# Optimization experiments

Hardware: AMD Instinct MI355X
Metric: run time of the kernel (lower is better)

Reference implementation:

```python
import jax, jax.numpy as jnp
import numpy as np

D_MODEL = 1024
N_HEADS = 16
HEAD_DIM = D_MODEL // N_HEADS
BATCH = 4
SEQ = 2048


def setup_inputs() -> dict:
    key = jax.random.key(0)
    ks = jax.random.split(key, 5)
    # Xavier uniform bound for square d_model x d_model weights
    bound = np.sqrt(6.0 / (D_MODEL + D_MODEL))
    x = jax.random.normal(ks[0], (BATCH, SEQ, D_MODEL), dtype=jnp.float32)
    attention_mask = jnp.ones((BATCH, SEQ), dtype=jnp.int32)
    wq = jax.random.uniform(ks[1], (D_MODEL, D_MODEL), jnp.float32, -bound, bound)
    wk = jax.random.uniform(ks[2], (D_MODEL, D_MODEL), jnp.float32, -bound, bound)
    wv = jax.random.uniform(ks[3], (D_MODEL, D_MODEL), jnp.float32, -bound, bound)
    wo = jax.random.uniform(ks[4], (D_MODEL, D_MODEL), jnp.float32, -bound, bound)
    return {"x": x, "attention_mask": attention_mask,
            "wq": wq, "wk": wk, "wv": wv, "wo": wo}


def reference(x, attention_mask, wq, wk, wv, wo):
    # x: (B, S, D). Linear weights stored torch-style (out, in): y = x @ W^T
    B, S, D = x.shape
    H, Hd = N_HEADS, HEAD_DIM
    scale = np.sqrt(Hd).astype(np.float32)

    def split_heads(t):  # (B,S,D) -> (B,H,S,Hd)
        return t.reshape(B, S, H, Hd).transpose(0, 2, 1, 3)

    q = split_heads(jnp.einsum('bsd,ed->bse', x, wq))
    k = split_heads(jnp.einsum('bsd,ed->bse', x, wk))
    v = split_heads(jnp.einsum('bsd,ed->bse', x, wv))

    scores = jnp.einsum('bhqd,bhkd->bhqk', q, k) / scale  # (B,H,S,S)

    causal = jnp.tril(jnp.ones((S, S), dtype=bool))  # True = keep
    keep = causal[None, None, :, :] & (attention_mask[:, None, None, :] != 0)
    scores = jnp.where(keep, scores, -jnp.inf)

    attn = jax.nn.softmax(scores, axis=-1)  # dropout: eval mode (identity)
    out = jnp.einsum('bhqk,bhkd->bhqd', attn, v)  # (B,H,S,Hd)
    out = out.transpose(0, 2, 1, 3).reshape(B, S, D)
    return jnp.einsum('bsd,ed->bse', out, wo)
```

## Files before the change

kernel.cpp:

```cpp
#include <hip/hip_runtime.h>
#include <cstdint>
#include <cstddef>

#define D_MODEL 1024
#define N_HEADS 16
#define HEAD_DIM 64
#define BATCH 4
#define SEQ 2048
#define M_TOTAL (BATCH * SEQ)

typedef __attribute__((ext_vector_type(8))) short bf16x8;
typedef __attribute__((ext_vector_type(4))) float f32x4;
typedef __attribute__((ext_vector_type(16))) float f32x16;

#define Q_SCALE 0.18033688011112042f

__device__ __forceinline__ unsigned short f2bu(float f) {
    union { float f; unsigned u; } x; x.f = f;
    unsigned r = x.u + 0x7FFFu + ((x.u >> 16) & 1u);
    return (unsigned short)(r >> 16);
}

__device__ __forceinline__ void async16(void* lds, const void* g) {
    __builtin_amdgcn_global_load_lds(
        (const __attribute__((address_space(1))) void*)g,
        (__attribute__((address_space(3))) void*)lds, 16, 0, 0);
}

__global__ __launch_bounds__(256) void cast_all(const float* __restrict__ x,
                                                const float* __restrict__ wq,
                                                const float* __restrict__ wk,
                                                const float* __restrict__ wv,
                                                const float* __restrict__ wo,
                                                unsigned short* __restrict__ dst) {
    const size_t NE = (size_t)M_TOTAL * D_MODEL;
    const size_t WE = (size_t)D_MODEL * D_MODEL;
    size_t i4 = (size_t)blockIdx.x * 256 + threadIdx.x;
    size_t e = i4 * 4;
    const float* src; size_t off;
    if (e < NE) { src = x; off = e; }
    else {
        size_t t = e - NE;
        int r = (int)(t / WE); off = t - (size_t)r * WE;
        src = (r == 0) ? wq : (r == 1) ? wk : (r == 2) ? wv : wo;
    }
    float4 v = *(const float4*)(src + off);
    ushort4 o;
    o.x = f2bu(v.x); o.y = f2bu(v.y); o.z = f2bu(v.z); o.w = f2bu(v.w);
    ((ushort4*)dst)[i4] = o;
}

__global__ __launch_bounds__(256) void qkv_gemm(const unsigned short* __restrict__ X,
                                                const unsigned short* __restrict__ W0,
                                                const unsigned short* __restrict__ W1,
                                                const unsigned short* __restrict__ W2,
                                                unsigned short* __restrict__ Y0,
                                                unsigned short* __restrict__ Y1,
                                                unsigned short* __restrict__ Vt) {
    __shared__ short As[128 * 32];
    __shared__ short Bs[128 * 32];

    const int sel = blockIdx.x >> 3;
    const unsigned short* W = (sel == 0) ? W0 : (sel == 1) ? W1 : W2;
    const float scl = (sel == 0) ? Q_SCALE : 1.0f;

    const int tid = threadIdx.x;
    const int w = tid >> 6, lane = tid & 63, quad = lane >> 4, l15 = lane & 15;
    const int wm = w & 1, wn = w >> 1;
    const int rowBase = blockIdx.y * 128;
    const int colBase = (blockIdx.x & 7) * 128;

    f32x4 acc[4][4];
#pragma unroll
    for (int mi = 0; mi < 4; ++mi)
#pragma unroll
        for (int ni = 0; ni < 4; ++ni)
#pragma unroll
            for (int e = 0; e < 4; ++e) acc[mi][ni][e] = 0.f;

    for (int k0 = 0; k0 < 1024; k0 += 32) {
        __syncthreads();
#pragma unroll
        for (int l = 0; l < 2; ++l) {
            int c = tid + l * 256;
            int row = c >> 2, ccs = c & 3;
            int cc = ccs ^ ((row >> 1) & 3);
            async16((char*)As + c * 16, X + (size_t)(rowBase + row) * 1024 + k0 + cc * 8);
            async16((char*)Bs + c * 16, W + (size_t)(colBase + row) * 1024 + k0 + cc * 8);
        }
        __syncthreads();

        bf16x8 a[4], b[4];
#pragma unroll
        for (int mi = 0; mi < 4; ++mi) {
            int r = wm * 64 + mi * 16 + l15;
            int slot = quad ^ ((r >> 1) & 3);
            a[mi] = *(const bf16x8*)&As[r * 32 + slot * 8];
        }
#pragma unroll
        for (int ni = 0; ni < 4; ++ni) {
            int r = wn * 64 + ni * 16 + l15;
            int slot = quad ^ ((r >> 1) & 3);
            b[ni] = *(const bf16x8*)&Bs[r * 32 + slot * 8];
        }
#pragma unroll
        for (int mi = 0; mi < 4; ++mi)
#pragma unroll
            for (int ni = 0; ni < 4; ++ni)
                acc[mi][ni] = __builtin_amdgcn_mfma_f32_16x16x32_bf16(a[mi], b[ni], acc[mi][ni], 0, 0, 0);
    }

    if (sel != 2) {
        unsigned short* Y = (sel == 0) ? Y0 : Y1;
#pragma unroll
        for (int mi = 0; mi < 4; ++mi)
#pragma unroll
            for (int ni = 0; ni < 4; ++ni)
#pragma unroll
                for (int reg = 0; reg < 4; ++reg) {
                    int row = rowBase + wm * 64 + mi * 16 + quad * 4 + reg;
                    int col = colBase + wn * 64 + ni * 16 + l15;
                    Y[(size_t)row * 1024 + col] = f2bu(acc[mi][ni][reg] * scl);
                }
    } else {
#pragma unroll
        for (int mi = 0; mi < 4; ++mi) {
            int row0 = rowBase + wm * 64 + mi * 16 + quad * 4;
            int bb = row0 >> 11;
            int s0 = row0 & 2047;
#pragma unroll
            for (int ni = 0; ni < 4; ++ni) {
                int col = colBase + wn * 64 + ni * 16 + l15;
                int hh = col >> 6, dd = col & 63;
                ushort4 pk;
                pk.x = f2bu(acc[mi][ni][0]); pk.y = f2bu(acc[mi][ni][1]);
                pk.z = f2bu(acc[mi][ni][2]); pk.w = f2bu(acc[mi][ni][3]);
                *(ushort4*)(Vt + (((size_t)bb * 16 + hh) * 64 + dd) * SEQ + s0) = pk;
            }
        }
    }
}

__global__ __launch_bounds__(256) void out_gemm(const unsigned short* __restrict__ X,
                                                const unsigned short* __restrict__ W,
                                                float* __restrict__ Y) {
    __shared__ short As[128 * 32];
    __shared__ short Bs[128 * 32];

    const int tid = threadIdx.x;
    const int w = tid >> 6, lane = tid & 63, quad = lane >> 4, l15 = lane & 15;
    const int wm = w & 1, wn = w >> 1;
    const int rowBase = blockIdx.y * 128;
    const int colBase = blockIdx.x * 128;

    f32x4 acc[4][4];
#pragma unroll
    for (int mi = 0; mi < 4; ++mi)
#pragma unroll
        for (int ni = 0; ni < 4; ++ni)
#pragma unroll
            for (int e = 0; e < 4; ++e) acc[mi][ni][e] = 0.f;

    for (int k0 = 0; k0 < 1024; k0 += 32) {
        __syncthreads();
#pragma unroll
        for (int l = 0; l < 2; ++l) {
            int c = tid + l * 256;
            int row = c >> 2, ccs = c & 3;
            int cc = ccs ^ ((row >> 1) & 3);
            async16((char*)As + c * 16, X + (size_t)(rowBase + row) * 1024 + k0 + cc * 8);
            async16((char*)Bs + c * 16, W + (size_t)(colBase + row) * 1024 + k0 + cc * 8);
        }
        __syncthreads();

        bf16x8 a[4], b[4];
#pragma unroll
        for (int mi = 0; mi < 4; ++mi) {
            int r = wm * 64 + mi * 16 + l15;
            int slot = quad ^ ((r >> 1) & 3);
            a[mi] = *(const bf16x8*)&As[r * 32 + slot * 8];
        }
#pragma unroll
        for (int ni = 0; ni < 4; ++ni) {
            int r = wn * 64 + ni * 16 + l15;
            int slot = quad ^ ((r >> 1) & 3);
            b[ni] = *(const bf16x8*)&Bs[r * 32 + slot * 8];
        }
#pragma unroll
        for (int mi = 0; mi < 4; ++mi)
#pragma unroll
            for (int ni = 0; ni < 4; ++ni)
                acc[mi][ni] = __builtin_amdgcn_mfma_f32_16x16x32_bf16(a[mi], b[ni], acc[mi][ni], 0, 0, 0);
    }

#pragma unroll
    for (int mi = 0; mi < 4; ++mi)
#pragma unroll
        for (int ni = 0; ni < 4; ++ni)
#pragma unroll
            for (int reg = 0; reg < 4; ++reg) {
                int row = rowBase + wm * 64 + mi * 16 + quad * 4 + reg;
                int col = colBase + wn * 64 + ni * 16 + l15;
                Y[(size_t)row * 1024 + col] = acc[mi][ni][reg];
            }
}

__global__ __launch_bounds__(256) void flash32(const unsigned short* __restrict__ Q,
                                               const unsigned short* __restrict__ K,
                                               const unsigned short* __restrict__ Vt,
                                               const int* __restrict__ mask,
                                               unsigned short* __restrict__ CTX) {
    __shared__ short lds[16384];
    __shared__ float biasS[2][64];
    __shared__ int allokS[2];
    __shared__ int okW[4];

    const int bh = blockIdx.x;
    const int qt = 15 - (int)blockIdx.y;
    const int b = bh >> 4;
    const int tid = threadIdx.x;
    const int w = tid >> 6, lane = tid & 63, l31 = lane & 31, lane5 = lane >> 5;

    const size_t qkBase = (size_t)b * SEQ * D_MODEL + (size_t)(bh & 15) * HEAD_DIM;
    const size_t vtBase = (size_t)bh * HEAD_DIM * SEQ;

    {
        int ok = 1;
        for (int i = tid; i < SEQ; i += 256) ok &= (mask[b * SEQ + i] != 0);
        unsigned long long bal = __ballot(ok != 0);
        if (lane == 0) okW[w] = (bal == ~0ull) ? 1 : 0;
    }
    __syncthreads();
    const int allSeq = okW[0] & okW[1] & okW[2] & okW[3];

    int stp[2], stcc[2], stj[2];
#pragma unroll
    for (int l = 0; l < 2; ++l) {
        int c = tid + l * 256;
        int p = c >> 3, sl = c & 7;
        stp[l] = p;
        stcc[l] = sl ^ (p & 7);
        stj[l] = (p & 0x33) | ((p & 4) << 1) | ((p & 8) >> 1);
    }

    const int q0 = qt * 128;
    const int iq = q0 + w * 32 + l31;

    bf16x8 qf[4];
#pragma unroll
    for (int ks = 0; ks < 4; ++ks)
        qf[ks] = *(const bf16x8*)(Q + qkBase + (size_t)iq * D_MODEL + ks * 16 + lane5 * 8);

    float mv = -INFINITY, lv = 0.f;
    f32x16 Ot[2];
#pragma unroll
    for (int dt = 0; dt < 2; ++dt)
#pragma unroll
        for (int e = 0; e < 16; ++e) Ot[dt][e] = 0.f;

    const int ktmax = 2 * qt + 1;

    uint4 kreg[2], vreg[2];
    int mreg = 1;
#pragma unroll
    for (int l = 0; l < 2; ++l) {
        kreg[l] = *(const uint4*)(K + qkBase + (size_t)stj[l] * D_MODEL + stcc[l] * 8);
        vreg[l] = *(const uint4*)(Vt + vtBase + (size_t)stp[l] * SEQ + stcc[l] * 8);
    }
    if (!allSeq && tid < 64) mreg = mask[b * SEQ + tid];

    for (int kt = 0; kt <= ktmax; ++kt) {
        const int k0 = kt * 64;
        const int buf = kt & 1;
#pragma unroll
        for (int l = 0; l < 2; ++l) {
            int c = tid + l * 256;
            *(uint4*)((char*)lds + buf * 8192 + c * 16) = kreg[l];
            *(uint4*)((char*)lds + 16384 + buf * 8192 + c * 16) = vreg[l];
        }
        if (!allSeq && tid < 64) {
            biasS[buf][tid] = mreg ? 0.f : -INFINITY;
            unsigned long long bal = __ballot(mreg != 0);
            if (tid == 0) allokS[buf] = (bal == ~0ull) ? 1 : 0;
        }
        if (kt < ktmax) {
            const int kn = k0 + 64;
#pragma unroll
            for (int l = 0; l < 2; ++l) {
                kreg[l] = *(const uint4*)(K + qkBase + (size_t)(kn + stj[l]) * D_MODEL + stcc[l] * 8);
                vreg[l] = *(const uint4*)(Vt + vtBase + (size_t)stp[l] * SEQ + kn + stcc[l] * 8);
            }
            if (!allSeq && tid < 64) mreg = mask[b * SEQ + kn + tid];
        }
        __syncthreads();

        if (64 * kt > q0 + 32 * w + 31) continue;

        const short* Ks = lds + buf * 4096;
        const short* Vs = lds + 8192 + buf * 4096;

        f32x16 St[2];
#pragma unroll
        for (int T = 0; T < 2; ++T)
#pragma unroll
            for (int e = 0; e < 16; ++e) St[T][e] = 0.f;
        __builtin_amdgcn_s_setprio(1);
#pragma unroll
        for (int T = 0; T < 2; ++T)
#pragma unroll
            for (int ks = 0; ks < 4; ++ks) {
                int p = T * 32 + l31;
                int slot = (ks * 2 + lane5) ^ (p & 7);
                bf16x8 a = *(const bf16x8*)&Ks[p * 64 + slot * 8];
                St[T] = __builtin_amdgcn_mfma_f32_32x32x16_bf16(a, qf[ks], St[T], 0, 0, 0);
            }
        __builtin_amdgcn_s_setprio(0);

        const bool partial = (k0 + 63 > q0 + 32 * w);
        if (partial) {
#pragma unroll
            for (int T = 0; T < 2; ++T)
#pragma unroll
                for (int r = 0; r < 16; ++r) {
                    int j = k0 + 32 * T + 16 * (r >> 3) + 8 * lane5 + (r & 7);
                    if (j > iq) St[T][r] = -INFINITY;
                }
        }
        if (!allSeq && !allokS[buf]) {
#pragma unroll
            for (int T = 0; T < 2; ++T)
#pragma unroll
                for (int r = 0; r < 16; ++r)
                    St[T][r] += biasS[buf][32 * T + 16 * (r >> 3) + 8 * lane5 + (r & 7)];
        }

        float t0[8];
#pragma unroll
        for (int r = 0; r < 8; ++r)
            t0[r] = fmaxf(fmaxf(St[0][r], St[0][r + 8]), fmaxf(St[1][r], St[1][r + 8]));
        float t1a = fmaxf(fmaxf(t0[0], t0[1]), fmaxf(t0[2], t0[3]));
        float t1b = fmaxf(fmaxf(t0[4], t0[5]), fmaxf(t0[6], t0[7]));
        float rm = fmaxf(t1a, t1b);
        rm = fmaxf(rm, __shfl_xor(rm, 32));
        float mn = fmaxf(mv, rm);
        if (mn > mv + 8.f) {
            float al = exp2f(mv - mn);
            lv *= al;
#pragma unroll
            for (int dt = 0; dt < 2; ++dt)
#pragma unroll
                for (int e = 0; e < 16; ++e) Ot[dt][e] *= al;
            mv = mn;
        }
        float rs = 0.f;
#pragma unroll
        for (int T = 0; T < 2; ++T)
#pragma unroll
            for (int r = 0; r < 16; ++r) {
                float pv = exp2f(St[T][r] - mv);
                St[T][r] = pv;
                rs += pv;
            }
        rs += __shfl_xor(rs, 32);
        lv += rs;

        bf16x8 pf[4];
#pragma unroll
        for (int t = 0; t < 4; ++t) {
            const int T = t >> 1, hb = t & 1;
            unsigned u0, u1, u2, u3;
            asm("v_cvt_pk_bf16_f32 %0, %1, %2" : "=v"(u0)
                : "v"(St[T][hb * 8 + 0]), "v"(St[T][hb * 8 + 1]));
            asm("v_cvt_pk_bf16_f32 %0, %1, %2" : "=v"(u1)
                : "v"(St[T][hb * 8 + 2]), "v"(St[T][hb * 8 + 3]));
            asm("v_cvt_pk_bf16_f32 %0, %1, %2" : "=v"(u2)
                : "v"(St[T][hb * 8 + 4]), "v"(St[T][hb * 8 + 5]));
            asm("v_cvt_pk_bf16_f32 %0, %1, %2" : "=v"(u3)
                : "v"(St[T][hb * 8 + 6]), "v"(St[T][hb * 8 + 7]));
            union { unsigned u[4]; bf16x8 v; } pk;
            pk.u[0] = u0; pk.u[1] = u1; pk.u[2] = u2; pk.u[3] = u3;
            pf[t] = pk.v;
        }

        __builtin_amdgcn_s_setprio(1);
#pragma unroll
        for (int dt = 0; dt < 2; ++dt)
#pragma unroll
            for (int t = 0; t < 4; ++t) {
                int p = dt * 32 + l31;
                int slot = (t * 2 + lane5) ^ (p & 7);
                bf16x8 a = *(const bf16x8*)&Vs[p * 64 + slot * 8];
                Ot[dt] = __builtin_amdgcn_mfma_f32_32x32x16_bf16(a, pf[t], Ot[dt], 0, 0, 0);
            }
        __builtin_amdgcn_s_setprio(0);
    }

    __syncthreads();
    const float inv = 1.f / lv;
#pragma unroll
    for (int dt = 0; dt < 2; ++dt)
#pragma unroll
        for (int k = 0; k < 8; ++k) {
            int r0 = 2 * k;
            int d = (r0 & 3) + 4 * lane5 + 8 * (r0 >> 2) + 32 * dt;
            unsigned lo = f2bu(Ot[dt][r0] * inv);
            unsigned hi = f2bu(Ot[dt][r0 + 1] * inv);
            *(unsigned*)&lds[(w * 32 + l31) * 72 + d] = lo | (hi << 16);
        }
    __syncthreads();
#pragma unroll
    for (int k = 0; k < 4; ++k) {
        int id = tid + k * 256;
        int r = id >> 3, cc = id & 7;
        uint4 v = *(const uint4*)&lds[r * 72 + cc * 8];
        *(uint4*)(CTX + qkBase + (size_t)(q0 + r) * D_MODEL + cc * 8) = v;
    }
}

extern "C" void kernel_launch(void* const* d_in, const int* in_sizes, int n_in,
                              void* d_out, int out_size, void* d_ws, size_t ws_size,
                              hipStream_t stream) {
    const float* x  = (const float*)d_in[0];
    const int* mask = (const int*)d_in[1];
    const float* wq = (const float*)d_in[2];
    const float* wk = (const float*)d_in[3];
    const float* wv = (const float*)d_in[4];
    const float* wo = (const float*)d_in[5];
    float* out = (float*)d_out;

    const size_t NE = (size_t)M_TOTAL * D_MODEL;
    const size_t WE = (size_t)D_MODEL * D_MODEL;
    unsigned short* ws  = (unsigned short*)d_ws;
    unsigned short* xb  = ws;
    unsigned short* wqb = xb + NE;
    unsigned short* wkb = wqb + WE;
    unsigned short* wvb = wkb + WE;
    unsigned short* wob = wvb + WE;
    unsigned short* Qb  = wob + WE;
    unsigned short* Kb  = Qb + NE;
    unsigned short* Vtb = Kb + NE;
    unsigned short* CTX = Vtb + NE;

    cast_all<<<(int)((NE + 4 * WE) / 4 / 256), 256, 0, stream>>>(x, wq, wk, wv, wo, ws);

    qkv_gemm<<<dim3(24, M_TOTAL / 128), 256, 0, stream>>>(xb, wqb, wkb, wvb, Qb, Kb, Vtb);

    flash32<<<dim3(64, 16), 256, 0, stream>>>(Qb, Kb, Vtb, mask, CTX);

    out_gemm<<<dim3(D_MODEL / 128, M_TOTAL / 128), 256, 0, stream>>>(CTX, wob, out);
}
```

Baseline: 326.7 us.

## Pair causal query tiles per block and widen KV tiles to 128 keys

Each flash-attention block now handles two query tiles (qt and 15-qt) in sequence, so every block does a similar amount of causal work, and the grid is halved. KV tiles grow from 64 to 128 keys, with a new V swizzle and LDS doubled to 64 KB, and diagonal tiles skip MFMAs for fully masked 32-key sub-blocks. This cuts loop iterations and barriers and evens out the load across blocks. In exchange it uses more LDS and registers, which may lower occupancy, and leaves fewer blocks to spread across the CUs.

```diff
diff --git a/kernel.cpp b/kernel.cpp
--- a/kernel.cpp
+++ b/kernel.cpp
@@ -210,13 +210,13 @@
                                                const unsigned short* __restrict__ Vt,
                                                const int* __restrict__ mask,
                                                unsigned short* __restrict__ CTX) {
-    __shared__ short lds[16384];
-    __shared__ float biasS[2][64];
-    __shared__ int allokS[2];
+    __shared__ short lds[32768];
+    __shared__ float biasS[2][128];
+    __shared__ int allokT[2][2];
     __shared__ int okW[4];
 
     const int bh = blockIdx.x;
-    const int qt = 15 - (int)blockIdx.y;
+    const int pid = blockIdx.y;
     const int b = bh >> 4;
     const int tid = threadIdx.x;
     const int w = tid >> 6, lane = tid & 63, l31 = lane & 31, lane5 = lane >> 5;
@@ -233,187 +233,211 @@
     __syncthreads();
     const int allSeq = okW[0] & okW[1] & okW[2] & okW[3];
 
-    int stp[2], stcc[2], stj[2];
-#pragma unroll
-    for (int l = 0; l < 2; ++l) {
+    int stcK[4], stjK[4], stpV[4], stcV[4];
+#pragma unroll
+    for (int l = 0; l < 4; ++l) {
         int c = tid + l * 256;
-        int p = c >> 3, sl = c & 7;
-        stp[l] = p;
-        stcc[l] = sl ^ (p & 7);
-        stj[l] = (p & 0x33) | ((p & 4) << 1) | ((p & 8) >> 1);
-    }
-
-    const int q0 = qt * 128;
-    const int iq = q0 + w * 32 + l31;
-
-    bf16x8 qf[4];
-#pragma unroll
-    for (int ks = 0; ks < 4; ++ks)
-        qf[ks] = *(const bf16x8*)(Q + qkBase + (size_t)iq * D_MODEL + ks * 16 + lane5 * 8);
-
-    float mv = -INFINITY, lv = 0.f;
-    f32x16 Ot[2];
-#pragma unroll
-    for (int dt = 0; dt < 2; ++dt)
-#pragma unroll
-        for (int e = 0; e < 16; ++e) Ot[dt][e] = 0.f;
-
-    const int ktmax = 2 * qt + 1;
-
-    uint4 kreg[2], vreg[2];
-    int mreg = 1;
-#pragma unroll
-    for (int l = 0; l < 2; ++l) {
-        kreg[l] = *(const uint4*)(K + qkBase + (size_t)stj[l] * D_MODEL + stcc[l] * 8);
-        vreg[l] = *(const uint4*)(Vt + vtBase + (size_t)stp[l] * SEQ + stcc[l] * 8);
-    }
-    if (!allSeq && tid < 64) mreg = mask[b * SEQ + tid];
-
-    for (int kt = 0; kt <= ktmax; ++kt) {
-        const int k0 = kt * 64;
-        const int buf = kt & 1;
-#pragma unroll
-        for (int l = 0; l < 2; ++l) {
-            int c = tid + l * 256;
-            *(uint4*)((char*)lds + buf * 8192 + c * 16) = kreg[l];
-            *(uint4*)((char*)lds + 16384 + buf * 8192 + c * 16) = vreg[l];
-        }
-        if (!allSeq && tid < 64) {
-            biasS[buf][tid] = mreg ? 0.f : -INFINITY;
-            unsigned long long bal = __ballot(mreg != 0);
-            if (tid == 0) allokS[buf] = (bal == ~0ull) ? 1 : 0;
-        }
-        if (kt < ktmax) {
-            const int kn = k0 + 64;
-#pragma unroll
-            for (int l = 0; l < 2; ++l) {
-                kreg[l] = *(const uint4*)(K + qkBase + (size_t)(kn + stj[l]) * D_MODEL + stcc[l] * 8);
-                vreg[l] = *(const uint4*)(Vt + vtBase + (size_t)stp[l] * SEQ + kn + stcc[l] * 8);
-            }
-            if (!allSeq && tid < 64) mreg = mask[b * SEQ + kn + tid];
-        }
-        __syncthreads();
-
-        if (64 * kt > q0 + 32 * w + 31) continue;
-
-        const short* Ks = lds + buf * 4096;
-        const short* Vs = lds + 8192 + buf * 4096;
-
-        f32x16 St[2];
-#pragma unroll
-        for (int T = 0; T < 2; ++T)
-#pragma unroll
-            for (int e = 0; e < 16; ++e) St[T][e] = 0.f;
-        __builtin_amdgcn_s_setprio(1);
-#pragma unroll
-        for (int T = 0; T < 2; ++T)
-#pragma unroll
-            for (int ks = 0; ks < 4; ++ks) {
-                int p = T * 32 + l31;
-                int slot = (ks * 2 + lane5) ^ (p & 7);
-                bf16x8 a = *(const bf16x8*)&Ks[p * 64 + slot * 8];
-                St[T] = __builtin_amdgcn_mfma_f32_32x32x16_bf16(a, qf[ks], St[T], 0, 0, 0);
-            }
-        __builtin_amdgcn_s_setprio(0);
-
-        const bool partial = (k0 + 63 > q0 + 32 * w);
-        if (partial) {
-#pragma unroll
-            for (int T = 0; T < 2; ++T)
-#pragma unroll
-                for (int r = 0; r < 16; ++r) {
-                    int j = k0 + 32 * T + 16 * (r >> 3) + 8 * lane5 + (r & 7);
-                    if (j > iq) St[T][r] = -INFINITY;
-                }
-        }
-        if (!allSeq && !allokS[buf]) {
-#pragma unroll
-            for (int T = 0; T < 2; ++T)
-#pragma unroll
-                for (int r = 0; r < 16; ++r)
-                    St[T][r] += biasS[buf][32 * T + 16 * (r >> 3) + 8 * lane5 + (r & 7)];
-        }
-
-        float t0[8];
-#pragma unroll
-        for (int r = 0; r < 8; ++r)
-            t0[r] = fmaxf(fmaxf(St[0][r], St[0][r + 8]), fmaxf(St[1][r], St[1][r + 8]));
-        float t1a = fmaxf(fmaxf(t0[0], t0[1]), fmaxf(t0[2], t0[3]));
-        float t1b = fmaxf(fmaxf(t0[4], t0[5]), fmaxf(t0[6], t0[7]));
-        float rm = fmaxf(t1a, t1b);
-        rm = fmaxf(rm, __shfl_xor(rm, 32));
-        float mn = fmaxf(mv, rm);
-        if (mn > mv + 8.f) {
-            float al = exp2f(mv - mn);
-            lv *= al;
+        int pK = c >> 3, slK = c & 7;
+        stcK[l] = slK ^ (pK & 7);
+        stjK[l] = (pK & 0xF3) | ((pK & 4) << 1) | ((pK & 8) >> 1);
+        int pV = c >> 4, slV = c & 15;
+        stpV[l] = pV;
+        stcV[l] = slV ^ (pV & 15);
+    }
+
+    for (int phase = 0; phase < 2; ++phase) {
+        const int qt = phase ? pid : 15 - pid;
+        const int q0 = qt * 128;
+        const int iq = q0 + w * 32 + l31;
+
+        bf16x8 qf[4];
+#pragma unroll
+        for (int ks = 0; ks < 4; ++ks)
+            qf[ks] = *(const bf16x8*)(Q + qkBase + (size_t)iq * D_MODEL + ks * 16 + lane5 * 8);
+
+        float mv = -INFINITY, lv = 0.f;
+        f32x16 Ot[2];
+#pragma unroll
+        for (int dt = 0; dt < 2; ++dt)
+#pragma unroll
+            for (int e = 0; e < 16; ++e) Ot[dt][e] = 0.f;
+
+        uint4 kreg[4], vreg[4];
+        int mreg = 1;
+#pragma unroll
+        for (int l = 0; l < 4; ++l) {
+            kreg[l] = *(const uint4*)(K + qkBase + (size_t)stjK[l] * D_MODEL + stcK[l] * 8);
+            vreg[l] = *(const uint4*)(Vt + vtBase + (size_t)stpV[l] * SEQ + stcV[l] * 8);
+        }
+        if (!allSeq && tid < 128) mreg = mask[b * SEQ + tid];
+
+        for (int kt = 0; kt <= qt; ++kt) {
+            const int k0 = kt * 128;
+            const int buf = kt & 1;
+            char* Kb = (char*)lds + buf * 16384;
+            char* Vb = (char*)lds + 32768 + buf * 16384;
+#pragma unroll
+            for (int l = 0; l < 4; ++l) {
+                int c = tid + l * 256;
+                *(uint4*)(Kb + c * 16) = kreg[l];
+                *(uint4*)(Vb + c * 16) = vreg[l];
+            }
+            if (!allSeq && tid < 128) {
+                biasS[buf][tid] = mreg ? 0.f : -INFINITY;
+                unsigned long long bal = __ballot(mreg != 0);
+                if (lane == 0) allokT[buf][w] = (bal == ~0ull) ? 1 : 0;
+            }
+            if (kt < qt) {
+                const int kn = k0 + 128;
+#pragma unroll
+                for (int l = 0; l < 4; ++l) {
+                    kreg[l] = *(const uint4*)(K + qkBase + (size_t)(kn + stjK[l]) * D_MODEL + stcK[l] * 8);
+                    vreg[l] = *(const uint4*)(Vt + vtBase + (size_t)stpV[l] * SEQ + kn + stcV[l] * 8);
+                }
+                if (!allSeq && tid < 128) mreg = mask[b * SEQ + kn + tid];
+            }
+            __syncthreads();
+
+            const short* Ks = (const short*)((char*)lds + buf * 16384);
+            const short* Vs = (const short*)((char*)lds + 32768 + buf * 16384);
+
+            const int kHi = q0 + 32 * w + 31 - k0;
+            const int nT = (kHi >> 5) >= 3 ? 4 : (kHi >> 5) + 1;
+            const int nt = (kHi >> 4) >= 7 ? 8 : (kHi >> 4) + 1;
+
+            f32x16 St[4];
+            __builtin_amdgcn_s_setprio(1);
+#pragma unroll
+            for (int T = 0; T < 4; ++T) {
+                if (T < nT) {
+#pragma unroll
+                    for (int e = 0; e < 16; ++e) St[T][e] = 0.f;
+#pragma unroll
+                    for (int ks = 0; ks < 4; ++ks) {
+                        int p = T * 32 + l31;
+                        int slot = (ks * 2 + lane5) ^ (p & 7);
+                        bf16x8 a = *(const bf16x8*)&Ks[p * 64 + slot * 8];
+                        St[T] = __builtin_amdgcn_mfma_f32_32x32x16_bf16(a, qf[ks], St[T], 0, 0, 0);
+                    }
+                }
+            }
+            __builtin_amdgcn_s_setprio(0);
+
+            if (kHi < 158) {
+#pragma unroll
+                for (int T = 0; T < 4; ++T)
+                    if (T < nT)
+#pragma unroll
+                        for (int r = 0; r < 16; ++r) {
+                            int j = k0 + 32 * T + 16 * (r >> 3) + 8 * lane5 + (r & 7);
+                            if (j > iq) St[T][r] = -INFINITY;
+                        }
+            }
+            if (!allSeq && !(allokT[buf][0] & allokT[buf][1])) {
+#pragma unroll
+                for (int T = 0; T < 4; ++T)
+                    if (T < nT)
+#pragma unroll
+                        for (int r = 0; r < 16; ++r)
+                            St[T][r] += biasS[buf][32 * T + 16 * (r >> 3) + 8 * lane5 + (r & 7)];
+            }
+
+            float tm[4];
+#pragma unroll
+            for (int T = 0; T < 4; ++T) {
+                if (T < nT) {
+                    float a0 = fmaxf(fmaxf(St[T][0], St[T][1]), fmaxf(St[T][2], St[T][3]));
+                    float a1 = fmaxf(fmaxf(St[T][4], St[T][5]), fmaxf(St[T][6], St[T][7]));
+                    float a2 = fmaxf(fmaxf(St[T][8], St[T][9]), fmaxf(St[T][10], St[T][11]));
+                    float a3 = fmaxf(fmaxf(St[T][12], St[T][13]), fmaxf(St[T][14], St[T][15]));
+                    tm[T] = fmaxf(fmaxf(a0, a1), fmaxf(a2, a3));
+                } else tm[T] = -INFINITY;
+            }
+            float rm = fmaxf(fmaxf(tm[0], tm[1]), fmaxf(tm[2], tm[3]));
+            rm = fmaxf(rm, __shfl_xor(rm, 32));
+            float mn = fmaxf(mv, rm);
+            if (mn > mv + 8.f) {
+                float al = exp2f(mv - mn);
+                lv *= al;
+#pragma unroll
+                for (int dt = 0; dt < 2; ++dt)
+#pragma unroll
+                    for (int e = 0; e < 16; ++e) Ot[dt][e] *= al;
+                mv = mn;
+            }
+            float rsp[4];
+#pragma unroll
+            for (int T = 0; T < 4; ++T) {
+                rsp[T] = 0.f;
+                if (T < nT) {
+#pragma unroll
+                    for (int r = 0; r < 16; ++r) {
+                        float pv = exp2f(St[T][r] - mv);
+                        St[T][r] = pv;
+                        rsp[T] += pv;
+                    }
+                }
+            }
+            float rs = (rsp[0] + rsp[1]) + (rsp[2] + rsp[3]);
+            rs += __shfl_xor(rs, 32);
+            lv += rs;
+
+            bf16x8 pf[8];
+#pragma unroll
+            for (int t = 0; t < 8; ++t) {
+                if (t < nt) {
+                    const int T = t >> 1, hb = t & 1;
+                    unsigned u0, u1, u2, u3;
+                    asm("v_cvt_pk_bf16_f32 %0, %1, %2" : "=v"(u0)
+                        : "v"(St[T][hb * 8 + 0]), "v"(St[T][hb * 8 + 1]));
+                    asm("v_cvt_pk_bf16_f32 %0, %1, %2" : "=v"(u1)
+                        : "v"(St[T][hb * 8 + 2]), "v"(St[T][hb * 8 + 3]));
+                    asm("v_cvt_pk_bf16_f32 %0, %1, %2" : "=v"(u2)
+                        : "v"(St[T][hb * 8 + 4]), "v"(St[T][hb * 8 + 5]));
+                    asm("v_cvt_pk_bf16_f32 %0, %1, %2" : "=v"(u3)
+                        : "v"(St[T][hb * 8 + 6]), "v"(St[T][hb * 8 + 7]));
+                    union { unsigned u[4]; bf16x8 v; } pk;
+                    pk.u[0] = u0; pk.u[1] = u1; pk.u[2] = u2; pk.u[3] = u3;
+                    pf[t] = pk.v;
+                }
+            }
+
+            __builtin_amdgcn_s_setprio(1);
 #pragma unroll
             for (int dt = 0; dt < 2; ++dt)
 #pragma unroll
-                for (int e = 0; e < 16; ++e) Ot[dt][e] *= al;
-            mv = mn;
-        }
-        float rs = 0.f;
-#pragma unroll
-        for (int T = 0; T < 2; ++T)
-#pragma unroll
-            for (int r = 0; r < 16; ++r) {
-                float pv = exp2f(St[T][r] - mv);
-                St[T][r] = pv;
-                rs += pv;
-            }
-        rs += __shfl_xor(rs, 32);
-        lv += rs;
-
-        bf16x8 pf[4];
-#pragma unroll
-        for (int t = 0; t < 4; ++t) {
-            const int T = t >> 1, hb = t & 1;
-            unsigned u0, u1, u2, u3;
-            asm("v_cvt_pk_bf16_f32 %0, %1, %2" : "=v"(u0)
-                : "v"(St[T][hb * 8 + 0]), "v"(St[T][hb * 8 + 1]));
-            asm("v_cvt_pk_bf16_f32 %0, %1, %2" : "=v"(u1)
-                : "v"(St[T][hb * 8 + 2]), "v"(St[T][hb * 8 + 3]));
-            asm("v_cvt_pk_bf16_f32 %0, %1, %2" : "=v"(u2)
-                : "v"(St[T][hb * 8 + 4]), "v"(St[T][hb * 8 + 5]));
-            asm("v_cvt_pk_bf16_f32 %0, %1, %2" : "=v"(u3)
-                : "v"(St[T][hb * 8 + 6]), "v"(St[T][hb * 8 + 7]));
-            union { unsigned u[4]; bf16x8 v; } pk;
-            pk.u[0] = u0; pk.u[1] = u1; pk.u[2] = u2; pk.u[3] = u3;
-            pf[t] = pk.v;
-        }
-
-        __builtin_amdgcn_s_setprio(1);
+                for (int t = 0; t < 8; ++t) {
+                    if (t < nt) {
+                        int p = dt * 32 + l31;
+                        int slot = (t * 2 + lane5) ^ (p & 15);
+                        bf16x8 a = *(const bf16x8*)&Vs[p * 128 + slot * 8];
+                        Ot[dt] = __builtin_amdgcn_mfma_f32_32x32x16_bf16(a, pf[t], Ot[dt], 0, 0, 0);
+                    }
+                }
+            __builtin_amdgcn_s_setprio(0);
+        }
+
+        __syncthreads();
+        const float inv = 1.f / lv;
 #pragma unroll
         for (int dt = 0; dt < 2; ++dt)
 #pragma unroll
-            for (int t = 0; t < 4; ++t) {
-                int p = dt * 32 + l31;
-                int slot = (t * 2 + lane5) ^ (p & 7);
-                bf16x8 a = *(const bf16x8*)&Vs[p * 64 + slot * 8];
-                Ot[dt] = __builtin_amdgcn_mfma_f32_32x32x16_bf16(a, pf[t], Ot[dt], 0, 0, 0);
-            }
-        __builtin_amdgcn_s_setprio(0);
-    }
-
-    __syncthreads();
-    const float inv = 1.f / lv;
-#pragma unroll
-    for (int dt = 0; dt < 2; ++dt)
-#pragma unroll
-        for (int k = 0; k < 8; ++k) {
-            int r0 = 2 * k;
-            int d = (r0 & 3) + 4 * lane5 + 8 * (r0 >> 2) + 32 * dt;
-            unsigned lo = f2bu(Ot[dt][r0] * inv);
-            unsigned hi = f2bu(Ot[dt][r0 + 1] * inv);
-            *(unsigned*)&lds[(w * 32 + l31) * 72 + d] = lo | (hi << 16);
-        }
-    __syncthreads();
-#pragma unroll
-    for (int k = 0; k < 4; ++k) {
-        int id = tid + k * 256;
-        int r = id >> 3, cc = id & 7;
-        uint4 v = *(const uint4*)&lds[r * 72 + cc * 8];
-        *(uint4*)(CTX + qkBase + (size_t)(q0 + r) * D_MODEL + cc * 8) = v;
+            for (int k = 0; k < 8; ++k) {
+                int r0 = 2 * k;
+                int d = (r0 & 3) + 4 * lane5 + 8 * (r0 >> 2) + 32 * dt;
+                unsigned lo = f2bu(Ot[dt][r0] * inv);
+                unsigned hi = f2bu(Ot[dt][r0 + 1] * inv);
+                *(unsigned*)&lds[(w * 32 + l31) * 72 + d] = lo | (hi << 16);
+            }
+        __syncthreads();
+#pragma unroll
+        for (int k = 0; k < 4; ++k) {
+            int id = tid + k * 256;
+            int r = id >> 3, cc = id & 7;
+            uint4 v = *(const uint4*)&lds[r * 72 + cc * 8];
+            *(uint4*)(CTX + qkBase + (size_t)(q0 + r) * D_MODEL + cc * 8) = v;
+        }
+        __syncthreads();
     }
 }
 
@@ -445,7 +469,7 @@
 
     qkv_gemm<<<dim3(24, M_TOTAL / 128), 256, 0, stream>>>(xb, wqb, wkb, wvb, Qb, Kb, Vtb);
 
-    flash32<<<dim3(64, 16), 256, 0, stream>>>(Qb, Kb, Vtb, mask, CTX);
+    flash32<<<dim3(64, 8), 256, 0, stream>>>(Qb, Kb, Vtb, mask, CTX);
 
     out_gemm<<<dim3(D_MODEL / 128, M_TOTAL / 128), 256, 0, stream>>>(CTX, wob, out);
 }
```

Result: slower. 436.2 us (+33.5%).

## Pair causal query tiles per block and skip fully-masked MFMA sub-tiles

Applied to the files above, without the earlier changes.

Each flash-attention block now processes two query tiles (15-pid and pid) in sequence, so every block does a balanced amount of causal work, and the grid is halved to 64x8. Inside the diagonal key tiles, the S=QK^T and PV MFMAs for 32- or 16-wide key sub-blocks that lie entirely above the diagonal are skipped via runtime nT/nt bounds. This targets load imbalance from the causal triangle and wasted MFMA work on masked regions, at the cost of fewer blocks in flight (512 blocks) and extra branching and register pressure in the inner loop.

```diff
diff --git a/kernel.cpp b/kernel.cpp
--- a/kernel.cpp
+++ b/kernel.cpp
@@ -216,7 +216,7 @@
     __shared__ int okW[4];
 
     const int bh = blockIdx.x;
-    const int qt = 15 - (int)blockIdx.y;
+    const int pid = blockIdx.y;
     const int b = bh >> 4;
     const int tid = threadIdx.x;
     const int w = tid >> 6, lane = tid & 63, l31 = lane & 31, lane5 = lane >> 5;
@@ -243,177 +243,201 @@
         stj[l] = (p & 0x33) | ((p & 4) << 1) | ((p & 8) >> 1);
     }
 
-    const int q0 = qt * 128;
-    const int iq = q0 + w * 32 + l31;
-
-    bf16x8 qf[4];
-#pragma unroll
-    for (int ks = 0; ks < 4; ++ks)
-        qf[ks] = *(const bf16x8*)(Q + qkBase + (size_t)iq * D_MODEL + ks * 16 + lane5 * 8);
-
-    float mv = -INFINITY, lv = 0.f;
-    f32x16 Ot[2];
-#pragma unroll
-    for (int dt = 0; dt < 2; ++dt)
-#pragma unroll
-        for (int e = 0; e < 16; ++e) Ot[dt][e] = 0.f;
-
-    const int ktmax = 2 * qt + 1;
-
-    uint4 kreg[2], vreg[2];
-    int mreg = 1;
-#pragma unroll
-    for (int l = 0; l < 2; ++l) {
-        kreg[l] = *(const uint4*)(K + qkBase + (size_t)stj[l] * D_MODEL + stcc[l] * 8);
-        vreg[l] = *(const uint4*)(Vt + vtBase + (size_t)stp[l] * SEQ + stcc[l] * 8);
-    }
-    if (!allSeq && tid < 64) mreg = mask[b * SEQ + tid];
-
-    for (int kt = 0; kt <= ktmax; ++kt) {
-        const int k0 = kt * 64;
-        const int buf = kt & 1;
+    for (int phase = 0; phase < 2; ++phase) {
+        const int qt = phase ? pid : 15 - pid;
+        const int q0 = qt * 128;
+        const int iq = q0 + w * 32 + l31;
+
+        bf16x8 qf[4];
+#pragma unroll
+        for (int ks = 0; ks < 4; ++ks)
+            qf[ks] = *(const bf16x8*)(Q + qkBase + (size_t)iq * D_MODEL + ks * 16 + lane5 * 8);
+
+        float mv = -INFINITY, lv = 0.f;
+        f32x16 Ot[2];
+#pragma unroll
+        for (int dt = 0; dt < 2; ++dt)
+#pragma unroll
+            for (int e = 0; e < 16; ++e) Ot[dt][e] = 0.f;
+
+        const int ktmax = 2 * qt + 1;
+
+        uint4 kreg[2], vreg[2];
+        int mreg = 1;
 #pragma unroll
         for (int l = 0; l < 2; ++l) {
-            int c = tid + l * 256;
-            *(uint4*)((char*)lds + buf * 8192 + c * 16) = kreg[l];
-            *(uint4*)((char*)lds + 16384 + buf * 8192 + c * 16) = vreg[l];
-        }
-        if (!allSeq && tid < 64) {
-            biasS[buf][tid] = mreg ? 0.f : -INFINITY;
-            unsigned long long bal = __ballot(mreg != 0);
-            if (tid == 0) allokS[buf] = (bal == ~0ull) ? 1 : 0;
-        }
-        if (kt < ktmax) {
-            const int kn = k0 + 64;
+            kreg[l] = *(const uint4*)(K + qkBase + (size_t)stj[l] * D_MODEL + stcc[l] * 8);
+            vreg[l] = *(const uint4*)(Vt + vtBase + (size_t)stp[l] * SEQ + stcc[l] * 8);
+        }
+        if (!allSeq && tid < 64) mreg = mask[b * SEQ + tid];
+
+        for (int kt = 0; kt <= ktmax; ++kt) {
+            const int k0 = kt * 64;
+            const int buf = kt & 1;
 #pragma unroll
             for (int l = 0; l < 2; ++l) {
-                kreg[l] = *(const uint4*)(K + qkBase + (size_t)(kn + stj[l]) * D_MODEL + stcc[l] * 8);
-                vreg[l] = *(const uint4*)(Vt + vtBase + (size_t)stp[l] * SEQ + kn + stcc[l] * 8);
-            }
-            if (!allSeq && tid < 64) mreg = mask[b * SEQ + kn + tid];
-        }
-        __syncthreads();
-
-        if (64 * kt > q0 + 32 * w + 31) continue;
-
-        const short* Ks = lds + buf * 4096;
-        const short* Vs = lds + 8192 + buf * 4096;
-
-        f32x16 St[2];
-#pragma unroll
-        for (int T = 0; T < 2; ++T)
-#pragma unroll
-            for (int e = 0; e < 16; ++e) St[T][e] = 0.f;
-        __builtin_amdgcn_s_setprio(1);
-#pragma unroll
-        for (int T = 0; T < 2; ++T)
-#pragma unroll
-            for (int ks = 0; ks < 4; ++ks) {
-                int p = T * 32 + l31;
-                int slot = (ks * 2 + lane5) ^ (p & 7);
-                bf16x8 a = *(const bf16x8*)&Ks[p * 64 + slot * 8];
-                St[T] = __builtin_amdgcn_mfma_f32_32x32x16_bf16(a, qf[ks], St[T], 0, 0, 0);
-            }
-        __builtin_amdgcn_s_setprio(0);
-
-        const bool partial = (k0 + 63 > q0 + 32 * w);
-        if (partial) {
-#pragma unroll
-            for (int T = 0; T < 2; ++T)
-#pragma unroll
-                for (int r = 0; r < 16; ++r) {
-                    int j = k0 + 32 * T + 16 * (r >> 3) + 8 * lane5 + (r & 7);
-                    if (j > iq) St[T][r] = -INFINITY;
-                }
-        }
-        if (!allSeq && !allokS[buf]) {
-#pragma unroll
-            for (int T = 0; T < 2; ++T)
-#pragma unroll
-                for (int r = 0; r < 16; ++r)
-                    St[T][r] += biasS[buf][32 * T + 16 * (r >> 3) + 8 * lane5 + (r & 7)];
-        }
-
-        float t0[8];
-#pragma unroll
-        for (int r = 0; r < 8; ++r)
-            t0[r] = fmaxf(fmaxf(St[0][r], St[0][r + 8]), fmaxf(St[1][r], St[1][r + 8]));
-        float t1a = fmaxf(fmaxf(t0[0], t0[1]), fmaxf(t0[2], t0[3]));
-        float t1b = fmaxf(fmaxf(t0[4], t0[5]), fmaxf(t0[6], t0[7]));
-        float rm = fmaxf(t1a, t1b);
-        rm = fmaxf(rm, __shfl_xor(rm, 32));
-        float mn = fmaxf(mv, rm);
-        if (mn > mv + 8.f) {
-            float al = exp2f(mv - mn);
-            lv *= al;
+                int c = tid + l * 256;
+                *(uint4*)((char*)lds + buf * 8192 + c * 16) = kreg[l];
+                *(uint4*)((char*)lds + 16384 + buf * 8192 + c * 16) = vreg[l];
+            }
+            if (!allSeq && tid < 64) {
+                biasS[buf][tid] = mreg ? 0.f : -INFINITY;
+                unsigned long long bal = __ballot(mreg != 0);
+                if (tid == 0) allokS[buf] = (bal == ~0ull) ? 1 : 0;
+            }
+            if (kt < ktmax) {
+                const int kn = k0 + 64;
+#pragma unroll
+                for (int l = 0; l < 2; ++l) {
+                    kreg[l] = *(const uint4*)(K + qkBase + (size_t)(kn + stj[l]) * D_MODEL + stcc[l] * 8);
+                    vreg[l] = *(const uint4*)(Vt + vtBase + (size_t)stp[l] * SEQ + kn + stcc[l] * 8);
+                }
+                if (!allSeq && tid < 64) mreg = mask[b * SEQ + kn + tid];
+            }
+            __syncthreads();
+
+            if (64 * kt > q0 + 32 * w + 31) continue;
+
+            const short* Ks = lds + buf * 4096;
+            const short* Vs = lds + 8192 + buf * 4096;
+
+            const int kHi = q0 + 32 * w + 31 - k0;
+            const int nT = (kHi >= 32) ? 2 : 1;
+            const int nt = ((kHi >> 4) >= 3 ? 3 : (kHi >> 4)) + 1;
+
+            f32x16 St[2];
+            __builtin_amdgcn_s_setprio(1);
+#pragma unroll
+            for (int T = 0; T < 2; ++T) {
+                if (T < nT) {
+#pragma unroll
+                    for (int e = 0; e < 16; ++e) St[T][e] = 0.f;
+#pragma unroll
+                    for (int ks = 0; ks < 4; ++ks) {
+                        int p = T * 32 + l31;
+                        int slot = (ks * 2 + lane5) ^ (p & 7);
+                        bf16x8 a = *(const bf16x8*)&Ks[p * 64 + slot * 8];
+                        St[T] = __builtin_amdgcn_mfma_f32_32x32x16_bf16(a, qf[ks], St[T], 0, 0, 0);
+                    }
+                }
+            }
+            __builtin_amdgcn_s_setprio(0);
+
+            const bool partial = (k0 + 63 > q0 + 32 * w);
+            if (partial) {
+#pragma unroll
+                for (int T = 0; T < 2; ++T)
+                    if (T < nT)
+#pragma unroll
+                        for (int r = 0; r < 16; ++r) {
+                            int j = k0 + 32 * T + 16 * (r >> 3) + 8 * lane5 + (r & 7);
+                            if (j > iq) St[T][r] = -INFINITY;
+                        }
+            }
+            if (!allSeq && !allokS[buf]) {
+#pragma unroll
+                for (int T = 0; T < 2; ++T)
+                    if (T < nT)
+#pragma unroll
+                        for (int r = 0; r < 16; ++r)
+                            St[T][r] += biasS[buf][32 * T + 16 * (r >> 3) + 8 * lane5 + (r & 7)];
+            }
+
+            float tm[2];
+#pragma unroll
+            for (int T = 0; T < 2; ++T) {
+                if (T < nT) {
+                    float a0 = fmaxf(fmaxf(St[T][0], St[T][1]), fmaxf(St[T][2], St[T][3]));
+                    float a1 = fmaxf(fmaxf(St[T][4], St[T][5]), fmaxf(St[T][6], St[T][7]));
+                    float a2 = fmaxf(fmaxf(St[T][8], St[T][9]), fmaxf(St[T][10], St[T][11]));
+                    float a3 = fmaxf(fmaxf(St[T][12], St[T][13]), fmaxf(St[T][14], St[T][15]));
+                    tm[T] = fmaxf(fmaxf(a0, a1), fmaxf(a2, a3));
+                } else tm[T] = -INFINITY;
+            }
+            float rm = fmaxf(tm[0], tm[1]);
+            rm = fmaxf(rm, __shfl_xor(rm, 32));
+            float mn = fmaxf(mv, rm);
+            if (mn > mv + 8.f) {
+                float al = exp2f(mv - mn);
+                lv *= al;
+#pragma unroll
+                for (int dt = 0; dt < 2; ++dt)
+#pragma unroll
+                    for (int e = 0; e < 16; ++e) Ot[dt][e] *= al;
+                mv = mn;
+            }
+            float rsp[2] = {0.f, 0.f};
+#pragma unroll
+            for (int T = 0; T < 2; ++T) {
+                if (T < nT) {
+#pragma unroll
+                    for (int r = 0; r < 16; ++r) {
+                        float pv = exp2f(St[T][r] - mv);
+                        St[T][r] = pv;
+                        rsp[T] += pv;
+                    }
+                }
+            }
+            float rs = rsp[0] + rsp[1];
+            rs += __shfl_xor(rs, 32);
+            lv += rs;
+
+            bf16x8 pf[4];
+#pragma unroll
+            for (int t = 0; t < 4; ++t) {
+                if (t < nt) {
+                    const int T = t >> 1, hb = t & 1;
+                    unsigned u0, u1, u2, u3;
+                    asm("v_cvt_pk_bf16_f32 %0, %1, %2" : "=v"(u0)
+                        : "v"(St[T][hb * 8 + 0]), "v"(St[T][hb * 8 + 1]));
+                    asm("v_cvt_pk_bf16_f32 %0, %1, %2" : "=v"(u1)
+                        : "v"(St[T][hb * 8 + 2]), "v"(St[T][hb * 8 + 3]));
+                    asm("v_cvt_pk_bf16_f32 %0, %1, %2" : "=v"(u2)
+                        : "v"(St[T][hb * 8 + 4]), "v"(St[T][hb * 8 + 5]));
+                    asm("v_cvt_pk_bf16_f32 %0, %1, %2" : "=v"(u3)
+                        : "v"(St[T][hb * 8 + 6]), "v"(St[T][hb * 8 + 7]));
+                    union { unsigned u[4]; bf16x8 v; } pk;
+                    pk.u[0] = u0; pk.u[1] = u1; pk.u[2] = u2; pk.u[3] = u3;
+                    pf[t] = pk.v;
+                }
+            }
+
+            __builtin_amdgcn_s_setprio(1);
 #pragma unroll
             for (int dt = 0; dt < 2; ++dt)
 #pragma unroll
-                for (int e = 0; e < 16; ++e) Ot[dt][e] *= al;
-            mv = mn;
-        }
-        float rs = 0.f;
-#pragma unroll
-        for (int T = 0; T < 2; ++T)
-#pragma unroll
-            for (int r = 0; r < 16; ++r) {
-                float pv = exp2f(St[T][r] - mv);
-                St[T][r] = pv;
-                rs += pv;
-            }
-        rs += __shfl_xor(rs, 32);
-        lv += rs;
-
-        bf16x8 pf[4];
-#pragma unroll
-        for (int t = 0; t < 4; ++t) {
-            const int T = t >> 1, hb = t & 1;
-            unsigned u0, u1, u2, u3;
-            asm("v_cvt_pk_bf16_f32 %0, %1, %2" : "=v"(u0)
-                : "v"(St[T][hb * 8 + 0]), "v"(St[T][hb * 8 + 1]));
-            asm("v_cvt_pk_bf16_f32 %0, %1, %2" : "=v"(u1)
-                : "v"(St[T][hb * 8 + 2]), "v"(St[T][hb * 8 + 3]));
-            asm("v_cvt_pk_bf16_f32 %0, %1, %2" : "=v"(u2)
-                : "v"(St[T][hb * 8 + 4]), "v"(St[T][hb * 8 + 5]));
-            asm("v_cvt_pk_bf16_f32 %0, %1, %2" : "=v"(u3)
-                : "v"(St[T][hb * 8 + 6]), "v"(St[T][hb * 8 + 7]));
-            union { unsigned u[4]; bf16x8 v; } pk;
-            pk.u[0] = u0; pk.u[1] = u1; pk.u[2] = u2; pk.u[3] = u3;
-            pf[t] = pk.v;
-        }
-
-        __builtin_amdgcn_s_setprio(1);
+                for (int t = 0; t < 4; ++t) {
+                    if (t < nt) {
+                        int p = dt * 32 + l31;
+                        int slot = (t * 2 + lane5) ^ (p & 7);
+                        bf16x8 a = *(const bf16x8*)&Vs[p * 64 + slot * 8];
+                        Ot[dt] = __builtin_amdgcn_mfma_f32_32x32x16_bf16(a, pf[t], Ot[dt], 0, 0, 0);
+                    }
+                }
+            __builtin_amdgcn_s_setprio(0);
+        }
+
+        __syncthreads();
+        const float inv = 1.f / lv;
 #pragma unroll
         for (int dt = 0; dt < 2; ++dt)
 #pragma unroll
-            for (int t = 0; t < 4; ++t) {
-                int p = dt * 32 + l31;
-                int slot = (t * 2 + lane5) ^ (p & 7);
-                bf16x8 a = *(const bf16x8*)&Vs[p * 64 + slot * 8];
-                Ot[dt] = __builtin_amdgcn_mfma_f32_32x32x16_bf16(a, pf[t], Ot[dt], 0, 0, 0);
-            }
-        __builtin_amdgcn_s_setprio(0);
-    }
-
-    __syncthreads();
-    const float inv = 1.f / lv;
-#pragma unroll
-    for (int dt = 0; dt < 2; ++dt)
-#pragma unroll
-        for (int k = 0; k < 8; ++k) {
-            int r0 = 2 * k;
-            int d = (r0 & 3) + 4 * lane5 + 8 * (r0 >> 2) + 32 * dt;
-            unsigned lo = f2bu(Ot[dt][r0] * inv);
-            unsigned hi = f2bu(Ot[dt][r0 + 1] * inv);
-            *(unsigned*)&lds[(w * 32 + l31) * 72 + d] = lo | (hi << 16);
-        }
-    __syncthreads();
-#pragma unroll
-    for (int k = 0; k < 4; ++k) {
-        int id = tid + k * 256;
-        int r = id >> 3, cc = id & 7;
-        uint4 v = *(const uint4*)&lds[r * 72 + cc * 8];
-        *(uint4*)(CTX + qkBase + (size_t)(q0 + r) * D_MODEL + cc * 8) = v;
+            for (int k = 0; k < 8; ++k) {
+                int r0 = 2 * k;
+                int d = (r0 & 3) + 4 * lane5 + 8 * (r0 >> 2) + 32 * dt;
+                unsigned lo = f2bu(Ot[dt][r0] * inv);
+                unsigned hi = f2bu(Ot[dt][r0 + 1] * inv);
+                *(unsigned*)&lds[(w * 32 + l31) * 72 + d] = lo | (hi << 16);
+            }
+        __syncthreads();
+#pragma unroll
+        for (int k = 0; k < 4; ++k) {
+            int id = tid + k * 256;
+            int r = id >> 3, cc = id & 7;
+            uint4 v = *(const uint4*)&lds[r * 72 + cc * 8];
+            *(uint4*)(CTX + qkBase + (size_t)(q0 + r) * D_MODEL + cc * 8) = v;
+        }
+        __syncthreads();
     }
 }
 
@@ -445,7 +469,7 @@
 
     qkv_gemm<<<dim3(24, M_TOTAL / 128), 256, 0, stream>>>(xb, wqb, wkb, wvb, Qb, Kb, Vtb);
 
-    flash32<<<dim3(64, 16), 256, 0, stream>>>(Qb, Kb, Vtb, mask, CTX);
+    flash32<<<dim3(64, 8), 256, 0, stream>>>(Qb, Kb, Vtb, mask, CTX);
 
     out_gemm<<<dim3(D_MODEL / 128, M_TOTAL / 128), 256, 0, stream>>>(CTX, wob, out);
 }
```

Result: faster. 309.7 us (-5.2%).
